# Optimization experiments

Hardware: AMD Instinct MI355X
Metric: run time of the kernel (lower is better)

The kernel has to match this reference:

```python
import math
import jax, jax.numpy as jnp
import numpy as np

B, N, D = 8, 2048, 512


def setup_inputs() -> dict:
    key = jax.random.key(0)
    ks = jax.random.split(key, 9)
    s = 1.0 / math.sqrt(D)
    return {
        "x": jax.random.normal(ks[0], (B, N, D), dtype=jnp.float32),
        "adj": jax.random.uniform(ks[1], (B, N, N), dtype=jnp.float32),
        "Wqk": jax.random.normal(ks[2], (D, D), dtype=jnp.float32) * s,
        "bqk": jax.random.normal(ks[3], (D,), dtype=jnp.float32) * s,
        "Wl": jax.random.normal(ks[4], (D, D), dtype=jnp.float32) * s,
        "bl": jax.random.normal(ks[5], (D,), dtype=jnp.float32) * s,
        "Wr": jax.random.normal(ks[6], (D, D), dtype=jnp.float32) * s,
        "Wd": jax.random.normal(ks[7], (D, 1), dtype=jnp.float32),
        "bd": jax.random.normal(ks[8], (D,), dtype=jnp.float32),
    }


def reference(x, adj, Wqk, bqk, Wl, bl, Wr, Wd, bd):
    # degree gating: sigmoid(Linear(rowsum(adj)))
    deg = jnp.sum(adj, axis=-1, keepdims=True)           # [B, N, 1]
    gate = jax.nn.sigmoid(deg * Wd[:, 0] + bd)           # [B, N, D]
    xg = x * gate
    # sigmoid QK features
    QK = jax.nn.sigmoid(xg @ Wqk.T + bqk)                # [B, N, D]
    scores = jnp.einsum("bnd,bmd->bnm", QK, QK) / math.sqrt(D)
    scores = scores * adj                                # adjacency mask
    attn = scores / (jnp.sum(scores, axis=-1, keepdims=True) + 1e-6)
    out = jnp.einsum("bnm,bmd->bnd", attn, xg)           # aggregate values
    out = out @ Wl.T + bl + xg @ Wr.T                    # left + right branch
    return jax.nn.relu(out)
```

## Files before the change

kernel.cpp:

```cpp
#include <hip/hip_runtime.h>
#include <hip/hip_bf16.h>


typedef __bf16 bf16;
typedef __bf16 bf16x2 __attribute__((ext_vector_type(2)));
typedef __bf16 bf16x8 __attribute__((ext_vector_type(8)));
typedef float  f32x4  __attribute__((ext_vector_type(4)));

#define Bb 8
#define Nn 2048
#define Dd 512
#define TILE8_BYTES 49152
#define SMEM8_BYTES (3 * TILE8_BYTES)
#define ATTN_SMEM (65536 + 33792 + 2048 + 256)

__device__ __forceinline__ bf16 to_bf16(float f) { return (bf16)f; }
__device__ __forceinline__ float sigmoidf_(float x) { return 1.0f / (1.0f + __expf(-x)); }

__device__ __forceinline__ void gld16(const void* g, void* l) {
    __builtin_amdgcn_global_load_lds(
        (__attribute__((address_space(1))) void*)(void*)g,
        (__attribute__((address_space(3))) void*)l,
        16, 0, 0);
}

__device__ __forceinline__ void gemm_bt8_core(
    const bf16* __restrict__ A0, const bf16* __restrict__ B0,
    int lda0, int ldb0, int nt0,
    const bf16* __restrict__ A1, const bf16* __restrict__ B1,
    int lda1, int ldb1, int nt1,
    char* smem, f32x4 acc[4][4])
{
    const int tid  = threadIdx.x;
    const int lane = tid & 63;
    const int wave = tid >> 6;
    const int wm = (wave >> 1) << 6;
    const int wn = (wave & 1) << 6;
    const int NT = nt0 + nt1;

    char* bA = smem;
    char* bB = smem + TILE8_BYTES;
    char* bC = smem + 2 * TILE8_BYTES;

    auto stage_tile = [&](char* base, int t) {
        const bf16* A  = (t < nt0) ? A0 : A1;
        const bf16* Bt = (t < nt0) ? B0 : B1;
        const int lda  = (t < nt0) ? lda0 : lda1;
        const int ldb  = (t < nt0) ? ldb0 : ldb1;
        const int kt   = ((t < nt0) ? t : t - nt0) << 6;
#pragma unroll
        for (int i = 0; i < 4; ++i) {
            int ff   = i * 512 + tid;
            int row  = ff >> 3;
            int slot = ff & 7;
            int gch  = slot ^ (row & 7);
            gld16(A + (size_t)row * lda + kt + gch * 8, base + ff * 16);
        }
#pragma unroll
        for (int i = 0; i < 2; ++i) {
            int ff   = i * 512 + tid;
            int row  = ff >> 3;
            int slot = ff & 7;
            int gch  = slot ^ (row & 7);
            gld16(Bt + (size_t)row * ldb + kt + gch * 8, base + 32768 + ff * 16);
        }
    };

    stage_tile(bA, 0);
    stage_tile(bB, 1);
    asm volatile("s_waitcnt vmcnt(6)" ::: "memory");
    __builtin_amdgcn_s_barrier();

#pragma unroll 1
    for (int t = 0; t < NT; ++t) {
        bf16x8 af0[4], bf0[4], af1[4], bf1[4];
#pragma unroll
        for (int mi = 0; mi < 4; ++mi) {
            int row  = wm + mi * 16 + (lane & 15);
            int slot = (lane >> 4) ^ (row & 7);
            af0[mi] = *(const bf16x8*)(bA + row * 128 + slot * 16);
        }
#pragma unroll
        for (int ni = 0; ni < 4; ++ni) {
            int row  = wn + ni * 16 + (lane & 15);
            int slot = (lane >> 4) ^ (row & 7);
            bf0[ni] = *(const bf16x8*)(bA + 32768 + row * 128 + slot * 16);
        }
        if (t + 2 < NT) stage_tile(bC, t + 2);
        __builtin_amdgcn_s_barrier();
        asm volatile("s_waitcnt lgkmcnt(0)" ::: "memory");
        __builtin_amdgcn_sched_barrier(0);
#pragma unroll
        for (int mi = 0; mi < 4; ++mi) {
            int row  = wm + mi * 16 + (lane & 15);
            int slot = (4 + (lane >> 4)) ^ (row & 7);
            af1[mi] = *(const bf16x8*)(bA + row * 128 + slot * 16);
        }
#pragma unroll
        for (int ni = 0; ni < 4; ++ni) {
            int row  = wn + ni * 16 + (lane & 15);
            int slot = (4 + (lane >> 4)) ^ (row & 7);
            bf1[ni] = *(const bf16x8*)(bA + 32768 + row * 128 + slot * 16);
        }
        __builtin_amdgcn_sched_barrier(0);
        __builtin_amdgcn_s_setprio(1);
#pragma unroll
        for (int mi = 0; mi < 4; ++mi)
#pragma unroll
            for (int ni = 0; ni < 4; ++ni)
                acc[mi][ni] = __builtin_amdgcn_mfma_f32_16x16x32_bf16(
                    af0[mi], bf0[ni], acc[mi][ni], 0, 0, 0);
        __builtin_amdgcn_s_setprio(0);
        asm volatile("s_waitcnt lgkmcnt(0)" ::: "memory");
        __builtin_amdgcn_sched_barrier(0);
        __builtin_amdgcn_s_setprio(1);
#pragma unroll
        for (int mi = 0; mi < 4; ++mi)
#pragma unroll
            for (int ni = 0; ni < 4; ++ni)
                acc[mi][ni] = __builtin_amdgcn_mfma_f32_16x16x32_bf16(
                    af1[mi], bf1[ni], acc[mi][ni], 0, 0, 0);
        __builtin_amdgcn_s_setprio(0);
        __builtin_amdgcn_sched_barrier(0);
        if (t + 2 < NT)      asm volatile("s_waitcnt vmcnt(6)" ::: "memory");
        else if (t + 1 < NT) asm volatile("s_waitcnt vmcnt(0)" ::: "memory");
        __builtin_amdgcn_s_barrier();
        char* tmp = bA; bA = bB; bB = bC; bC = tmp;
    }
}

template <typename F>
__device__ __forceinline__ void epilogue_rt8(f32x4 acc[4][4], char* smem, F&& emit)
{
    const int tid  = threadIdx.x;
    const int lane = tid & 63;
    const int wave = tid >> 6;
    const int wm4 = wave >> 1;
    const int wn  = (wave & 1) << 6;
    const int cq = lane >> 4;
    const int cl = lane & 15;
    float* t = (float*)smem;
    const int chunk = tid & 15;
    const int rbase = tid >> 4;
#pragma unroll
    for (int ph = 0; ph < 4; ++ph) {
        __syncthreads();
        if (wm4 == ph) {
#pragma unroll
            for (int mi = 0; mi < 4; ++mi)
#pragma unroll
                for (int ni = 0; ni < 4; ++ni)
#pragma unroll
                    for (int r = 0; r < 4; ++r) {
                        int lr = mi * 16 + cq * 4 + r;
                        int lc = wn + ni * 16 + cl;
                        t[lr * 132 + lc] = acc[mi][ni][r];
                    }
        }
        __syncthreads();
#pragma unroll
        for (int rr = 0; rr < 2; ++rr) {
            int lr = rr * 32 + rbase;
            f32x4 a = *(const f32x4*)&t[lr * 132 + chunk * 8];
            f32x4 b = *(const f32x4*)&t[lr * 132 + chunk * 8 + 4];
            float v[8] = {a[0], a[1], a[2], a[3], b[0], b[1], b[2], b[3]};
            emit(ph * 64 + lr, chunk * 8, v);
        }
    }
}

__global__ __launch_bounds__(256) void k_gate(
    const float* __restrict__ x, const float* __restrict__ adj,
    const float* __restrict__ Wd, const float* __restrict__ bd,
    const float* __restrict__ Wqk, const float* __restrict__ Wl,
    const float* __restrict__ Wr,
    bf16* __restrict__ xg, bf16* __restrict__ Wqkb, bf16* __restrict__ Wlb,
    bf16* __restrict__ Wrb)
{
    const int rowg = blockIdx.x;
    const int tid  = threadIdx.x;
    if (tid < 48) {
        int idx = rowg * 48 + tid;
        if (idx < 262144)      Wqkb[idx]          = to_bf16(Wqk[idx]);
        else if (idx < 524288) Wlb[idx - 262144]  = to_bf16(Wl[idx - 262144]);
        else                   Wrb[idx - 524288]  = to_bf16(Wr[idx - 524288]);
    }

    const float4* arow = (const float4*)(adj + (size_t)rowg * Nn);
    float4 v0 = arow[tid];
    float4 v1 = arow[tid + 256];
    float s = v0.x + v0.y + v0.z + v0.w + v1.x + v1.y + v1.z + v1.w;
#pragma unroll
    for (int off = 32; off > 0; off >>= 1) s += __shfl_down(s, off, 64);
    __shared__ float red[4];
    if ((tid & 63) == 0) red[tid >> 6] = s;
    __syncthreads();
    const float deg = red[0] + red[1] + red[2] + red[3];
    const int d2 = tid;
    float2 xv  = ((const float2*)(x + (size_t)rowg * Dd))[d2];
    float2 wd  = ((const float2*)Wd)[d2];
    float2 bd2 = ((const float2*)bd)[d2];
    bf16x2 o;
    o[0] = to_bf16(xv.x * sigmoidf_(deg * wd.x + bd2.x));
    o[1] = to_bf16(xv.y * sigmoidf_(deg * wd.y + bd2.y));
    *(bf16x2*)(xg + (size_t)rowg * Dd + d2 * 2) = o;
}

__global__ __launch_bounds__(256) void k_transpose(
    const bf16* __restrict__ xg, bf16* __restrict__ xgT)
{
    const int b = blockIdx.z, nt = blockIdx.y, dt = blockIdx.x;
    __shared__ bf16 tile[64][66];
    const int c = threadIdx.x & 63, r0 = threadIdx.x >> 6;
    const bf16* src = xg + ((size_t)b * Nn + nt * 64) * Dd + dt * 64;
#pragma unroll
    for (int i = 0; i < 16; ++i) {
        int r = i * 4 + r0;
        tile[r][c] = src[(size_t)r * Dd + c];
    }
    __syncthreads();
    bf16* dst = xgT + ((size_t)b * Dd + dt * 64) * Nn + nt * 64;
#pragma unroll
    for (int i = 0; i < 16; ++i) {
        int r = i * 4 + r0;
        dst[(size_t)r * Nn + c] = tile[c][r];
    }
}

__global__ __launch_bounds__(512) void k_qk_gemm8(
    const bf16* __restrict__ xg, const bf16* __restrict__ Wqkb,
    const float* __restrict__ bqk, bf16* __restrict__ QK)
{
    extern __shared__ __align__(16) char smem[];
    const int blockRow = blockIdx.y * 256;
    const int blockCol = blockIdx.x * 128;
    f32x4 acc[4][4];
#pragma unroll
    for (int mi = 0; mi < 4; ++mi)
#pragma unroll
        for (int ni = 0; ni < 4; ++ni) acc[mi][ni] = (f32x4){0.f, 0.f, 0.f, 0.f};
    gemm_bt8_core(xg + (size_t)blockRow * Dd, Wqkb + (size_t)blockCol * Dd,
                  Dd, Dd, 8,
                  xg, Wqkb, Dd, Dd, 0, smem, acc);
    epilogue_rt8(acc, smem, [&](int lr, int lc, float* v) {
        int c = blockCol + lc;
        float4 b0 = *(const float4*)(bqk + c);
        float4 b1 = *(const float4*)(bqk + c + 4);
        float bb[8] = {b0.x, b0.y, b0.z, b0.w, b1.x, b1.y, b1.z, b1.w};
        bf16x8 o;
#pragma unroll
        for (int j = 0; j < 8; ++j) o[j] = to_bf16(sigmoidf_(v[j] + bb[j]));
        *(bf16x8*)(QK + (size_t)(blockRow + lr) * Dd + c) = o;
    });
}

__global__ __launch_bounds__(512) void k_attn(
    const bf16* __restrict__ QK, const bf16* __restrict__ xgT,
    const float* __restrict__ adj, bf16* __restrict__ h)
{
    extern __shared__ __align__(16) char smem[];
    char*  qki  = smem;
    char*  Pl   = smem + 65536;
    float* dred = (float*)(smem + 65536 + 33792);
    float* dinv = (float*)(smem + 65536 + 33792 + 2048);

    const int id   = blockIdx.x;
    const int b    = id & 7;
    const int row0 = (id >> 3) * 64;
    const int tid  = threadIdx.x;
    const int lane = tid & 63, w = tid >> 6;
    const int cq = lane >> 4, cl = lane & 15;

    const bf16*  QKb  = QK  + (size_t)b * Nn * Dd;
    const bf16*  QKi  = QKb + (size_t)row0 * Dd;
    const bf16*  xgTb = xgT + (size_t)b * Dd * Nn;
    const float* adjb = adj + (size_t)b * Nn * Nn + (size_t)row0 * Nn;

#pragma unroll
    for (int i = 0; i < 8; ++i) {
        int ff = i * 512 + tid;
        int row = ff >> 6, slot = ff & 63;
        int gch = (slot & 56) | ((slot & 7) ^ (row & 7));
        gld16(QKi + (size_t)row * Dd + gch * 8, qki + ff * 16);
    }

    f32x4 hacc[4][4];
#pragma unroll
    for (int mi = 0; mi < 4; ++mi)
#pragma unroll
        for (int ni = 0; ni < 4; ++ni) hacc[mi][ni] = (f32x4){0.f, 0.f, 0.f, 0.f};
    float dloc[16];
#pragma unroll
    for (int i = 0; i < 16; ++i) dloc[i] = 0.f;
    float acur[2][16];

    __syncthreads();

    const float scale = 0.044194173824159216f;

#pragma unroll 1
    for (int jt = 0; jt < 8; ++jt) {
        const int j0 = jt * 256;
#pragma unroll
        for (int nf = 0; nf < 2; ++nf)
#pragma unroll
            for (int mi = 0; mi < 4; ++mi)
#pragma unroll
                for (int r = 0; r < 4; ++r)
                    acur[nf][mi * 4 + r] =
                        adjb[(size_t)(mi * 16 + cq * 4 + r) * Nn + j0 + w * 32 + nf * 16 + cl];

        f32x4 tacc[2][4];
#pragma unroll
        for (int nf = 0; nf < 2; ++nf)
#pragma unroll
            for (int mi = 0; mi < 4; ++mi) tacc[nf][mi] = (f32x4){0.f, 0.f, 0.f, 0.f};
#pragma unroll
        for (int kc = 0; kc < 16; ++kc) {
            bf16x8 af[4], bq[2];
#pragma unroll
            for (int nf = 0; nf < 2; ++nf)
                bq[nf] = *(const bf16x8*)(QKb
                    + (size_t)(j0 + w * 32 + nf * 16 + cl) * Dd + kc * 32 + cq * 8);
#pragma unroll
            for (int mi = 0; mi < 4; ++mi) {
                int row = mi * 16 + cl;
                int chunk = kc * 4 + cq;
                int slot = (chunk & 56) | ((chunk & 7) ^ (row & 7));
                af[mi] = *(const bf16x8*)(qki + row * 1024 + slot * 16);
            }
#pragma unroll
            for (int nf = 0; nf < 2; ++nf)
#pragma unroll
                for (int mi = 0; mi < 4; ++mi)
                    tacc[nf][mi] = __builtin_amdgcn_mfma_f32_16x16x32_bf16(
                        af[mi], bq[nf], tacc[nf][mi], 0, 0, 0);
        }
        __syncthreads();
#pragma unroll
        for (int nf = 0; nf < 2; ++nf)
#pragma unroll
            for (int mi = 0; mi < 4; ++mi)
#pragma unroll
                for (int r = 0; r < 4; ++r) {
                    float s = tacc[nf][mi][r] * scale * acur[nf][mi * 4 + r];
                    bf16 sb = to_bf16(s);
                    *(bf16*)(Pl + (mi * 16 + cq * 4 + r) * 528
                                + (w * 32 + nf * 16 + cl) * 2) = sb;
                    dloc[mi * 4 + r] += (float)sb;
                }
        __syncthreads();
#pragma unroll
        for (int kc = 0; kc < 8; ++kc) {
            bf16x8 pa[4], xb[4];
#pragma unroll
            for (int mi = 0; mi < 4; ++mi)
                pa[mi] = *(const bf16x8*)(Pl + (mi * 16 + cl) * 528 + kc * 64 + cq * 16);
#pragma unroll
            for (int ni = 0; ni < 4; ++ni)
                xb[ni] = *(const bf16x8*)(xgTb
                    + (size_t)(w * 64 + ni * 16 + cl) * Nn + j0 + kc * 32 + cq * 8);
#pragma unroll
            for (int mi = 0; mi < 4; ++mi)
#pragma unroll
                for (int ni = 0; ni < 4; ++ni)
                    hacc[mi][ni] = __builtin_amdgcn_mfma_f32_16x16x32_bf16(
                        pa[mi], xb[ni], hacc[mi][ni], 0, 0, 0);
        }
    }

#pragma unroll
    for (int i = 0; i < 16; ++i)
#pragma unroll
        for (int off = 1; off < 16; off <<= 1)
            dloc[i] += __shfl_xor(dloc[i], off, 64);
    if (cl == 0) {
#pragma unroll
        for (int mi = 0; mi < 4; ++mi)
#pragma unroll
            for (int r = 0; r < 4; ++r)
                dred[w * 64 + mi * 16 + cq * 4 + r] = dloc[mi * 4 + r];
    }
    __syncthreads();
    if (tid < 64) {
        float s = 0.f;
#pragma unroll
        for (int k = 0; k < 8; ++k) s += dred[k * 64 + tid];
        dinv[tid] = 1.0f / (s + 1e-6f);
    }
    __syncthreads();

    float* hs = (float*)smem;
#pragma unroll
    for (int p = 0; p < 2; ++p) {
        if (p) __syncthreads();
#pragma unroll
        for (int m2 = 0; m2 < 2; ++m2) {
            int mi = p * 2 + m2;
#pragma unroll
            for (int r = 0; r < 4; ++r) {
                float iv = dinv[mi * 16 + cq * 4 + r];
                int lrow = m2 * 16 + cq * 4 + r;
#pragma unroll
                for (int ni = 0; ni < 4; ++ni)
                    hs[lrow * 516 + w * 64 + ni * 16 + cl] = hacc[mi][ni][r] * iv;
            }
        }
        __syncthreads();
        {
            int row = tid & 31, ch = tid >> 5;
            int grow = row0 + p * 32 + row;
            bf16* dst = h + ((size_t)b * Nn + grow) * Dd + ch * 32;
            const float* src = hs + row * 516 + ch * 32;
#pragma unroll
            for (int g = 0; g < 4; ++g) {
                f32x4 u = *(const f32x4*)(src + g * 8);
                f32x4 q = *(const f32x4*)(src + g * 8 + 4);
                bf16x8 o;
                o[0] = to_bf16(u[0]); o[1] = to_bf16(u[1]);
                o[2] = to_bf16(u[2]); o[3] = to_bf16(u[3]);
                o[4] = to_bf16(q[0]); o[5] = to_bf16(q[1]);
                o[6] = to_bf16(q[2]); o[7] = to_bf16(q[3]);
                *(bf16x8*)(dst + g * 8) = o;
            }
        }
    }
}

__global__ __launch_bounds__(512) void k_out_gemm8(
    const bf16* __restrict__ h, const bf16* __restrict__ xg,
    const bf16* __restrict__ Wlb, const bf16* __restrict__ Wrb,
    const float* __restrict__ bl, float* __restrict__ out)
{
    extern __shared__ __align__(16) char smem[];
    const int blockRow = blockIdx.y * 256;
    const int blockCol = blockIdx.x * 128;
    f32x4 acc[4][4];
#pragma unroll
    for (int mi = 0; mi < 4; ++mi)
#pragma unroll
        for (int ni = 0; ni < 4; ++ni) acc[mi][ni] = (f32x4){0.f, 0.f, 0.f, 0.f};
    gemm_bt8_core(h  + (size_t)blockRow * Dd, Wlb + (size_t)blockCol * Dd,
                  Dd, Dd, 8,
                  xg + (size_t)blockRow * Dd, Wrb + (size_t)blockCol * Dd,
                  Dd, Dd, 8, smem, acc);
    epilogue_rt8(acc, smem, [&](int lr, int lc, float* v) {
        int c = blockCol + lc;
        float4 b0 = *(const float4*)(bl + c);
        float4 b1 = *(const float4*)(bl + c + 4);
        float bb[8] = {b0.x, b0.y, b0.z, b0.w, b1.x, b1.y, b1.z, b1.w};
        float4 o0, o1;
        o0.x = fmaxf(v[0] + bb[0], 0.f); o0.y = fmaxf(v[1] + bb[1], 0.f);
        o0.z = fmaxf(v[2] + bb[2], 0.f); o0.w = fmaxf(v[3] + bb[3], 0.f);
        o1.x = fmaxf(v[4] + bb[4], 0.f); o1.y = fmaxf(v[5] + bb[5], 0.f);
        o1.z = fmaxf(v[6] + bb[6], 0.f); o1.w = fmaxf(v[7] + bb[7], 0.f);
        float* p = out + (size_t)(blockRow + lr) * Dd + c;
        *(float4*)p = o0;
        *(float4*)(p + 4) = o1;
    });
}

extern "C" void kernel_launch(void* const* d_in, const int* in_sizes, int n_in,
                              void* d_out, int out_size, void* d_ws, size_t ws_size,
                              hipStream_t stream) {
    const float* x   = (const float*)d_in[0];
    const float* adj = (const float*)d_in[1];
    const float* Wqk = (const float*)d_in[2];
    const float* bqk = (const float*)d_in[3];
    const float* Wl  = (const float*)d_in[4];
    const float* bl  = (const float*)d_in[5];
    const float* Wr  = (const float*)d_in[6];
    const float* Wd  = (const float*)d_in[7];
    const float* bd  = (const float*)d_in[8];
    float* out = (float*)d_out;

    char* ws = (char*)d_ws;
    bf16* xg   = (bf16*)ws;  ws += (size_t)Bb * Nn * Dd * 2;
    bf16* xgT  = (bf16*)ws;  ws += (size_t)Bb * Dd * Nn * 2;
    bf16* QK   = (bf16*)ws;  ws += (size_t)Bb * Nn * Dd * 2;
    bf16* h    = (bf16*)ws;  ws += (size_t)Bb * Nn * Dd * 2;
    bf16* Wqkb = (bf16*)ws;  ws += (size_t)Dd * Dd * 2;
    bf16* Wlb  = (bf16*)ws;  ws += (size_t)Dd * Dd * 2;
    bf16* Wrb  = (bf16*)ws;  ws += (size_t)Dd * Dd * 2;

    static bool attr_done = false;
    if (!attr_done) {
        hipFuncSetAttribute((const void*)k_qk_gemm8,
                            hipFuncAttributeMaxDynamicSharedMemorySize, SMEM8_BYTES);
        hipFuncSetAttribute((const void*)k_attn,
                            hipFuncAttributeMaxDynamicSharedMemorySize, ATTN_SMEM);
        hipFuncSetAttribute((const void*)k_out_gemm8,
                            hipFuncAttributeMaxDynamicSharedMemorySize, SMEM8_BYTES);
        attr_done = true;
    }

    k_gate<<<dim3(Bb * Nn), 256, 0, stream>>>(x, adj, Wd, bd, Wqk, Wl, Wr,
                                              xg, Wqkb, Wlb, Wrb);
    k_transpose<<<dim3(Dd / 64, Nn / 64, Bb), 256, 0, stream>>>(xg, xgT);
    k_qk_gemm8<<<dim3(Dd / 128, (Bb * Nn) / 256), 512, SMEM8_BYTES, stream>>>(xg, Wqkb, bqk, QK);
    k_attn<<<dim3(256), 512, ATTN_SMEM, stream>>>(QK, xgT, adj, h);
    k_out_gemm8<<<dim3(Dd / 128, (Bb * Nn) / 256), 512, SMEM8_BYTES, stream>>>(h, xg, Wlb, Wrb, bl, out);
}
```

Before: 430.8 us.

## Double-buffer adjacency tiles in LDS via async loads and halve key tile width

The attention kernel now stages the adjacency tile into shared memory with async global-to-LDS loads, double-buffered so the next tile's fetch overlaps the current tile's compute. Previously each thread read adjacency values straight from global memory before the score MFMAs. The key tile shrinks from 256 to 128 columns, which cuts registers and the P buffer size, and P now uses an XOR-swizzled layout. Launch bounds request two blocks per CU. The cost is a larger LDS footprint of 144KB, which may prevent two blocks from fitting per CU, and twice as many loop iterations, each with its own barriers.

After: 440.0 us. 2.1% more time.

```diff
diff --git a/kernel.cpp b/kernel.cpp
--- a/kernel.cpp
+++ b/kernel.cpp
@@ -12,7 +12,7 @@
 #define Dd 512
 #define TILE8_BYTES 49152
 #define SMEM8_BYTES (3 * TILE8_BYTES)
-#define ATTN_SMEM (65536 + 33792 + 2048 + 256)
+#define ATTN_SMEM 147456
 
 __device__ __forceinline__ bf16 to_bf16(float f) { return (bf16)f; }
 __device__ __forceinline__ float sigmoidf_(float x) { return 1.0f / (1.0f + __expf(-x)); }
@@ -254,15 +254,17 @@
     });
 }
 
-__global__ __launch_bounds__(512) void k_attn(
+__global__ __launch_bounds__(512, 2) void k_attn(
     const bf16* __restrict__ QK, const bf16* __restrict__ xgT,
     const float* __restrict__ adj, bf16* __restrict__ h)
 {
     extern __shared__ __align__(16) char smem[];
-    char*  qki  = smem;
-    char*  Pl   = smem + 65536;
-    float* dred = (float*)(smem + 65536 + 33792);
-    float* dinv = (float*)(smem + 65536 + 33792 + 2048);
+    char* qki = smem;
+    char* Pl  = smem + 65536;
+    char* adj0 = smem + 81920;
+    char* adj1 = smem + 114688;
+    float* dred = (float*)adj0;
+    float* dinv = (float*)(adj0 + 2048);
 
     const int id   = blockIdx.x;
     const int b    = id & 7;
@@ -276,6 +278,17 @@
     const bf16*  xgTb = xgT + (size_t)b * Dd * Nn;
     const float* adjb = adj + (size_t)b * Nn * Nn + (size_t)row0 * Nn;
 
+    auto stage_adj = [&](char* base, int jt) {
+        const int j0 = jt << 7;
+#pragma unroll
+        for (int i = 0; i < 4; ++i) {
+            int ff  = i * 512 + tid;
+            int row = ff >> 5, slot = ff & 31;
+            int gch = (slot & 24) | ((slot & 7) ^ (row & 7));
+            gld16(adjb + (size_t)row * Nn + j0 + gch * 4, base + ff * 16);
+        }
+    };
+
 #pragma unroll
     for (int i = 0; i < 8; ++i) {
         int ff = i * 512 + tid;
@@ -283,6 +296,7 @@
         int gch = (slot & 56) | ((slot & 7) ^ (row & 7));
         gld16(QKi + (size_t)row * Dd + gch * 8, qki + ff * 16);
     }
+    stage_adj(adj0, 0);
 
     f32x4 hacc[4][4];
 #pragma unroll
@@ -292,70 +306,67 @@
     float dloc[16];
 #pragma unroll
     for (int i = 0; i < 16; ++i) dloc[i] = 0.f;
-    float acur[2][16];
 
     __syncthreads();
 
     const float scale = 0.044194173824159216f;
 
 #pragma unroll 1
-    for (int jt = 0; jt < 8; ++jt) {
-        const int j0 = jt * 256;
-#pragma unroll
-        for (int nf = 0; nf < 2; ++nf)
+    for (int jt = 0; jt < 16; ++jt) {
+        const int j0 = jt << 7;
+        f32x4 tacc[4];
+#pragma unroll
+        for (int mi = 0; mi < 4; ++mi) tacc[mi] = (f32x4){0.f, 0.f, 0.f, 0.f};
+#pragma unroll
+        for (int kc = 0; kc < 16; ++kc) {
+            bf16x8 bq = *(const bf16x8*)(QKb
+                + (size_t)(j0 + w * 16 + cl) * Dd + kc * 32 + cq * 8);
+            bf16x8 af[4];
+#pragma unroll
+            for (int mi = 0; mi < 4; ++mi) {
+                int i = mi * 16 + cl;
+                int c = kc * 4 + cq;
+                int ph = (c & 56) | ((c & 7) ^ (i & 7));
+                af[mi] = *(const bf16x8*)(qki + i * 1024 + ph * 16);
+            }
 #pragma unroll
             for (int mi = 0; mi < 4; ++mi)
-#pragma unroll
-                for (int r = 0; r < 4; ++r)
-                    acur[nf][mi * 4 + r] =
-                        adjb[(size_t)(mi * 16 + cq * 4 + r) * Nn + j0 + w * 32 + nf * 16 + cl];
-
-        f32x4 tacc[2][4];
-#pragma unroll
-        for (int nf = 0; nf < 2; ++nf)
-#pragma unroll
-            for (int mi = 0; mi < 4; ++mi) tacc[nf][mi] = (f32x4){0.f, 0.f, 0.f, 0.f};
-#pragma unroll
-        for (int kc = 0; kc < 16; ++kc) {
-            bf16x8 af[4], bq[2];
-#pragma unroll
-            for (int nf = 0; nf < 2; ++nf)
-                bq[nf] = *(const bf16x8*)(QKb
-                    + (size_t)(j0 + w * 32 + nf * 16 + cl) * Dd + kc * 32 + cq * 8);
+                tacc[mi] = __builtin_amdgcn_mfma_f32_16x16x32_bf16(
+                    af[mi], bq, tacc[mi], 0, 0, 0);
+        }
+        __syncthreads();
+
+        const char* ab = (jt & 1) ? adj1 : adj0;
+#pragma unroll
+        for (int mi = 0; mi < 4; ++mi)
+#pragma unroll
+            for (int r = 0; r < 4; ++r) {
+                int i = mi * 16 + cq * 4 + r;
+                int ca = w * 4 + (cl >> 2);
+                int pha = (ca & 24) | ((ca & 7) ^ (i & 7));
+                float a = *(const float*)(ab + i * 512 + pha * 16 + (cl & 3) * 4);
+                float s = tacc[mi][r] * scale * a;
+                bf16 sb = to_bf16(s);
+                int cj = w * 2 + (cl >> 3);
+                int phj = (cj & 8) | ((cj & 7) ^ (i & 7));
+                *(bf16*)(Pl + i * 256 + phj * 16 + (cl & 7) * 2) = sb;
+                dloc[mi * 4 + r] += (float)sb;
+            }
+        if (jt + 1 < 16) stage_adj((jt & 1) ? adj0 : adj1, jt + 1);
+        asm volatile("s_waitcnt lgkmcnt(0)" ::: "memory");
+        __builtin_amdgcn_sched_barrier(0);
+        __builtin_amdgcn_s_barrier();
+
+#pragma unroll
+        for (int kc = 0; kc < 4; ++kc) {
+            bf16x8 pa[4], xb[4];
 #pragma unroll
             for (int mi = 0; mi < 4; ++mi) {
-                int row = mi * 16 + cl;
-                int chunk = kc * 4 + cq;
-                int slot = (chunk & 56) | ((chunk & 7) ^ (row & 7));
-                af[mi] = *(const bf16x8*)(qki + row * 1024 + slot * 16);
+                int i = mi * 16 + cl;
+                int c = kc * 4 + cq;
+                int ph = (c & 8) | ((c & 7) ^ (i & 7));
+                pa[mi] = *(const bf16x8*)(Pl + i * 256 + ph * 16);
             }
-#pragma unroll
-            for (int nf = 0; nf < 2; ++nf)
-#pragma unroll
-                for (int mi = 0; mi < 4; ++mi)
-                    tacc[nf][mi] = __builtin_amdgcn_mfma_f32_16x16x32_bf16(
-                        af[mi], bq[nf], tacc[nf][mi], 0, 0, 0);
-        }
-        __syncthreads();
-#pragma unroll
-        for (int nf = 0; nf < 2; ++nf)
-#pragma unroll
-            for (int mi = 0; mi < 4; ++mi)
-#pragma unroll
-                for (int r = 0; r < 4; ++r) {
-                    float s = tacc[nf][mi][r] * scale * acur[nf][mi * 4 + r];
-                    bf16 sb = to_bf16(s);
-                    *(bf16*)(Pl + (mi * 16 + cq * 4 + r) * 528
-                                + (w * 32 + nf * 16 + cl) * 2) = sb;
-                    dloc[mi * 4 + r] += (float)sb;
-                }
-        __syncthreads();
-#pragma unroll
-        for (int kc = 0; kc < 8; ++kc) {
-            bf16x8 pa[4], xb[4];
-#pragma unroll
-            for (int mi = 0; mi < 4; ++mi)
-                pa[mi] = *(const bf16x8*)(Pl + (mi * 16 + cl) * 528 + kc * 64 + cq * 16);
 #pragma unroll
             for (int ni = 0; ni < 4; ++ni)
                 xb[ni] = *(const bf16x8*)(xgTb
```
